# Kernel tuning notes

Hardware: AMD Instinct MI355X
Metric: run time of the kernel (lower is better)

The kernel has to match this reference:

```python
import jax, jax.numpy as jnp
import numpy as np

B, N, C, H, K = 16, 1024, 384, 6, 8
HID = int(C * 2.0)  # mlp_ratio = 2.0
HD = C // H


def _layernorm(x, w, b, eps=1e-5):
    m = x.mean(-1, keepdims=True)
    v = ((x - m) ** 2).mean(-1, keepdims=True)
    return (x - m) * jax.lax.rsqrt(v + eps) * w + b


def setup_inputs() -> dict:
    key = jax.random.key(0)
    ks = jax.random.split(key, 16)
    x = jax.random.normal(ks[0], (B, N, C), jnp.float32)
    # knn indices within each batch, offset by batch*N (as in get_knn_index)
    idx = jax.random.randint(ks[1], (B, K, N), 0, N)
    base = jnp.arange(B, dtype=jnp.int32)[:, None, None] * N
    knn_index = (idx + base).reshape(-1).astype(jnp.int32)
    s = 0.02
    p = {
        "x": x,
        "knn_index": knn_index,
        "ln1_w": jnp.ones((C,), jnp.float32),
        "ln1_b": jnp.zeros((C,), jnp.float32),
        "w_qkv": jax.random.normal(ks[2], (C, 3 * C), jnp.float32) * s,  # qkv_bias=False
        "w_proj": jax.random.normal(ks[3], (C, C), jnp.float32) * s,
        "b_proj": jnp.zeros((C,), jnp.float32),
        "w_knn": jax.random.normal(ks[4], (2 * C, C), jnp.float32) * s,
        "b_knn": jnp.zeros((C,), jnp.float32),
        "w_merge": jax.random.normal(ks[5], (2 * C, C), jnp.float32) * s,
        "b_merge": jnp.zeros((C,), jnp.float32),
        "ln2_w": jnp.ones((C,), jnp.float32),
        "ln2_b": jnp.zeros((C,), jnp.float32),
        "w_fc1": jax.random.normal(ks[6], (C, HID), jnp.float32) * s,
        "b_fc1": jnp.zeros((HID,), jnp.float32),
        "w_fc2": jax.random.normal(ks[7], (HID, C), jnp.float32) * s,
        "b_fc2": jnp.zeros((C,), jnp.float32),
    }
    return p


def reference(x, knn_index, ln1_w, ln1_b, w_qkv, w_proj, b_proj, w_knn, b_knn,
              w_merge, b_merge, ln2_w, ln2_b, w_fc1, b_fc1, w_fc2, b_fc2):
    nx = _layernorm(x, ln1_w, ln1_b)  # [B,N,C]

    # --- self attention ---
    qkv = (nx @ w_qkv).reshape(B, N, 3, H, HD)
    q, k, v = qkv[:, :, 0], qkv[:, :, 1], qkv[:, :, 2]  # [B,N,H,HD]
    scale = HD ** (-0.5)
    attn = jnp.einsum("bnhd,bmhd->bhnm", q, k) * scale
    attn = jax.nn.softmax(attn, axis=-1)
    a_out = jnp.einsum("bhnm,bmhd->bnhd", attn, v).reshape(B, N, C)
    x1 = a_out @ w_proj + b_proj

    # --- graph feature: gather, relative concat, Linear+LeakyReLU, max over k ---
    feat = nx.reshape(B * N, C)[knn_index].reshape(B, K, N, C)
    center = nx[:, None, :, :]  # [B,1,N,C]
    g = jnp.concatenate([feat - center, jnp.broadcast_to(center, (B, K, N, C))], axis=-1)
    knn_f = jax.nn.leaky_relu(g @ w_knn + b_knn, negative_slope=0.2)
    knn_f = knn_f.max(axis=1)  # [B,N,C]

    x1 = jnp.concatenate([x1, knn_f], axis=-1) @ w_merge + b_merge
    x = x + x1

    # --- MLP ---
    h = _layernorm(x, ln2_w, ln2_b)
    h = jax.nn.gelu(h @ w_fc1 + b_fc1, approximate=False) @ w_fc2 + b_fc2
    return x + h
```

## Files before the change

kernel.cpp:

```cpp
#include <hip/hip_runtime.h>
#include <hip/hip_bf16.h>
#include <math.h>

#define BN_ROWS 16384
#define CDIM 384
#define NH 6
#define BBATCH 16
#define NNN 1024

typedef unsigned short u16;
typedef unsigned int u32;
typedef __attribute__((ext_vector_type(8))) short short8;
typedef __attribute__((ext_vector_type(4))) float floatx4;

__device__ __forceinline__ float b2f(u16 s) { return __uint_as_float(((u32)s) << 16); }
__device__ __forceinline__ u16 f2b(float f) {
    __hip_bfloat16 h = __float2bfloat16(f);
    u16 s; __builtin_memcpy(&s, &h, 2); return s;
}
__device__ __forceinline__ void gload_lds16(const u16* g, u16* l) {
    __builtin_amdgcn_global_load_lds(
        (const __attribute__((address_space(1))) unsigned int*)g,
        (__attribute__((address_space(3))) unsigned int*)l, 16, 0, 0);
}

__global__ __launch_bounds__(256) void pack_all(
    const float* __restrict__ W0, u16* __restrict__ T0,
    const float* __restrict__ W1, u16* __restrict__ T1,
    const float* __restrict__ W2, u16* __restrict__ T2,
    const float* __restrict__ W3, u16* __restrict__ T3,
    const float* __restrict__ W4, u16* __restrict__ T4,
    const float* __restrict__ W5, u16* __restrict__ T5)
{
    const float* W; u16* T; int K, N;
    switch (blockIdx.z) {
        case 0: W = W0; T = T0; K = 384; N = 1152; break;
        case 1: W = W1; T = T1; K = 384; N = 384;  break;
        case 2: W = W2; T = T2; K = 768; N = 384;  break;
        case 3: W = W3; T = T3; K = 768; N = 384;  break;
        case 4: W = W4; T = T4; K = 384; N = 768;  break;
        default: W = W5; T = T5; K = 768; N = 384; break;
    }
    const int n0 = blockIdx.x * 32, k0 = blockIdx.y * 32;
    if (n0 >= N || k0 >= K) return;
    __shared__ float s[32][33];
    const int tx = threadIdx.x & 31, ty = threadIdx.x >> 5;
#pragma unroll
    for (int i = 0; i < 4; ++i)
        s[ty + 8 * i][tx] = W[(size_t)(k0 + ty + 8 * i) * N + n0 + tx];
    __syncthreads();
#pragma unroll
    for (int i = 0; i < 4; ++i)
        T[(size_t)(n0 + ty + 8 * i) * K + k0 + tx] = f2b(s[tx][ty + 8 * i]);
}

__global__ __launch_bounds__(64) void ln_kernel(const float* __restrict__ xin,
                                                const float* __restrict__ w,
                                                const float* __restrict__ b,
                                                u16* __restrict__ out)
{
    const int row = blockIdx.x;
    const int t = threadIdx.x;
    const size_t base = (size_t)row * CDIM;
    float v[6];
#pragma unroll
    for (int i = 0; i < 6; ++i) v[i] = xin[base + t + 64 * i];
    float s = 0.f, s2 = 0.f;
#pragma unroll
    for (int i = 0; i < 6; ++i) { s += v[i]; s2 += v[i] * v[i]; }
#pragma unroll
    for (int m = 1; m < 64; m <<= 1) {
        s  += __shfl_xor(s,  m, 64);
        s2 += __shfl_xor(s2, m, 64);
    }
    const float mean = s * (1.0f / CDIM);
    const float var  = s2 * (1.0f / CDIM) - mean * mean;
    const float rs   = rsqrtf(var + 1e-5f);
#pragma unroll
    for (int i = 0; i < 6; ++i) {
        int c = t + 64 * i;
        out[base + c] = f2b((v[i] - mean) * rs * w[c] + b[c]);
    }
}

template<int ACT, bool HAS_BIAS, bool HAS_RES, bool OUT_F32, int MODE, int NT>
__global__ __launch_bounds__(256) void gemm_mfma_kernel(
    const u16* __restrict__ A, int lda,
    const u16* __restrict__ Bt, const u16* __restrict__ Bt2, int ldbt,
    u16* Cb, u16* Cb2, float* Cf, int ldc,
    const float* __restrict__ bias,
    const float* res,
    int K)
{
    constexpr int NTL = NT / 32;
    __shared__ u16 As[128 * 32];
    __shared__ u16 Bs[NT * 32];
    const int tid  = threadIdx.x;
    const int wv   = tid >> 6;
    const int lane = tid & 63;
    const int l15  = lane & 15;
    const int quad = lane >> 4;
    const int m0 = blockIdx.y * 128;
    const int n0 = blockIdx.x * NT;
    const int woffm = (wv >> 1) * 64;
    const int woffn = (wv & 1) * (NT / 2);

    const u16* bsrc = (MODE == 2 && n0 >= 384) ? Bt2 : Bt;
    const int  bn0  = (MODE == 2 && n0 >= 384) ? (n0 - 384) : n0;

    floatx4 acc[4][NTL];
#pragma unroll
    for (int mt = 0; mt < 4; ++mt)
#pragma unroll
        for (int nt = 0; nt < NTL; ++nt) acc[mt][nt] = (floatx4){0.f, 0.f, 0.f, 0.f};

    const int gsw  = 8 * ((lane & 3) ^ ((lane >> 3) & 3));
    const int rloc = lane >> 2;
    const int rdsw = 8 * (quad ^ ((l15 >> 1) & 3));

    for (int kt = 0; kt < K; kt += 32) {
#pragma unroll
        for (int j = 0; j < 2; ++j) {
            const int slab = 32 * wv + 16 * j;
            gload_lds16(A + (size_t)(m0 + slab + rloc) * lda + kt + gsw, &As[slab * 32]);
        }
        if (NT == 128) {
#pragma unroll
            for (int j = 0; j < 2; ++j) {
                const int slab = 32 * wv + 16 * j;
                gload_lds16(bsrc + (size_t)(bn0 + slab + rloc) * ldbt + kt + gsw, &Bs[slab * 32]);
            }
        } else {
            const int slab = 16 * wv;
            gload_lds16(bsrc + (size_t)(bn0 + slab + rloc) * ldbt + kt + gsw, &Bs[slab * 32]);
        }
        __syncthreads();

        short8 af[4], bf[NTL];
#pragma unroll
        for (int mt = 0; mt < 4; ++mt)
            af[mt] = *(const short8*)(As + (woffm + mt * 16 + l15) * 32 + rdsw);
#pragma unroll
        for (int nt = 0; nt < NTL; ++nt)
            bf[nt] = *(const short8*)(Bs + (woffn + nt * 16 + l15) * 32 + rdsw);
#pragma unroll
        for (int mt = 0; mt < 4; ++mt)
#pragma unroll
            for (int nt = 0; nt < NTL; ++nt)
                acc[mt][nt] = __builtin_amdgcn_mfma_f32_16x16x32_bf16(
                    af[mt], bf[nt], acc[mt][nt], 0, 0, 0);
        __syncthreads();
    }

#pragma unroll
    for (int nt = 0; nt < NTL; ++nt) {
        const int gc = n0 + woffn + nt * 16 + l15;
        float bi = 0.f;
        if (HAS_BIAS) bi = bias[gc];
        if (MODE == 2) bi = (gc >= 384) ? bias[gc - 384] : 0.f;
#pragma unroll
        for (int mt = 0; mt < 4; ++mt) {
            const int gr0 = m0 + woffm + mt * 16 + quad * 4;
#pragma unroll
            for (int rr = 0; rr < 4; ++rr) {
                float v = acc[mt][nt][rr] + bi;
                if (ACT == 1) v = 0.5f * v * (1.0f + erff(v * 0.70710678118654752f));
                if (HAS_RES)  v += res[(size_t)(gr0 + rr) * ldc + gc];
                if (MODE == 1) {
                    const int t3  = gc / 384;
                    const int rem = gc - t3 * 384;
                    const int hh = rem >> 6, dd = rem & 63;
                    const int bb = (gr0 + rr) >> 10, nn = (gr0 + rr) & 1023;
                    Cb[((size_t)((bb * 6 + hh) * 1024 + nn)) * 192 + t3 * 64 + dd] = f2b(v);
                } else if (MODE == 2) {
                    if (gc < 384) Cb [(size_t)(gr0 + rr) * 384 + gc]       = f2b(v);
                    else          Cb2[(size_t)(gr0 + rr) * 384 + gc - 384] = f2b(v);
                } else if (OUT_F32) {
                    Cf[(size_t)(gr0 + rr) * ldc + gc] = v;
                } else {
                    Cb[(size_t)(gr0 + rr) * ldc + gc] = f2b(v);
                }
            }
        }
    }
}

__global__ __launch_bounds__(256) void attn_mfma_kernel(const u16* __restrict__ qkv2,
                                                        u16* __restrict__ aout)
{
    const int id = blockIdx.x;
    const int rxcd = id & 7;
    const int j = id >> 3;
    const int slab = rxcd + 8 * (j % 12);
    const int qtile = j / 12;
    const int b = slab / NH, h = slab % NH;

    const int wave = threadIdx.x >> 6;
    const int lane = threadIdx.x & 63;
    const int l15 = lane & 15;
    const int quad = lane >> 4;
    const int qbase = qtile * 128 + wave * 32;
    const int tid = threadIdx.x;

    const u16* slabp = qkv2 + ((size_t)(b * NH + h) << 10) * 192;

    __shared__ __align__(16) u16 Ks[64 * 72];
    __shared__ __align__(16) u16 Vt[64 * 72];
    __shared__ __align__(16) u16 Ps[4][32 * 72];
    __shared__ __align__(16) float Ls[4][32];

    short8 qf[2][2];
#pragma unroll
    for (int nt = 0; nt < 2; ++nt) {
        const u16* qrow = slabp + (size_t)(qbase + nt * 16 + l15) * 192;
        qf[nt][0] = *(const short8*)(qrow + quad * 8);
        qf[nt][1] = *(const short8*)(qrow + 32 + quad * 8);
    }

    float rowsum[2] = {0.f, 0.f};
    floatx4 Oacc[2][4];
#pragma unroll
    for (int mt = 0; mt < 2; ++mt)
#pragma unroll
        for (int nt = 0; nt < 4; ++nt) Oacc[mt][nt] = (floatx4){0.f, 0.f, 0.f, 0.f};

    for (int kc = 0; kc < NNN; kc += 64) {
        {
            const int key = tid >> 2, dblk = (tid & 3) * 16;
            const u16* kp = slabp + (size_t)(kc + key) * 192 + 64 + dblk;
            *(short8*)(Ks + key * 72 + dblk)     = *(const short8*)(kp);
            *(short8*)(Ks + key * 72 + dblk + 8) = *(const short8*)(kp + 8);
        }
        {
            const int kp2 = tid & 31, db = (tid >> 5) * 8;
            const u16* v0p = slabp + (size_t)(kc + 2 * kp2) * 192 + 128 + db;
            uint4 v0 = *(const uint4*)(v0p);
            uint4 v1 = *(const uint4*)(v0p + 192);
            u32 a0[4] = {v0.x, v0.y, v0.z, v0.w};
            u32 a1[4] = {v1.x, v1.y, v1.z, v1.w};
#pragma unroll
            for (int i = 0; i < 8; ++i) {
                u32 w0 = (i & 1) ? (a0[i >> 1] >> 16) : (a0[i >> 1] & 0xffffu);
                u32 w1 = (i & 1) ? (a1[i >> 1] >> 16) : (a1[i >> 1] & 0xffffu);
                *(u32*)(Vt + (size_t)(db + i) * 72 + 2 * kp2) = w0 | (w1 << 16);
            }
        }
        __syncthreads();

        floatx4 sc[4][2];
#pragma unroll
        for (int kt_ = 0; kt_ < 4; ++kt_) {
            short8 kf0 = *(const short8*)(Ks + (kt_ * 16 + l15) * 72 + quad * 8);
            short8 kf1 = *(const short8*)(Ks + (kt_ * 16 + l15) * 72 + 32 + quad * 8);
#pragma unroll
            for (int nt = 0; nt < 2; ++nt) {
                floatx4 s = {0.f, 0.f, 0.f, 0.f};
                s = __builtin_amdgcn_mfma_f32_16x16x32_bf16(kf0, qf[nt][0], s, 0, 0, 0);
                s = __builtin_amdgcn_mfma_f32_16x16x32_bf16(kf1, qf[nt][1], s, 0, 0, 0);
                sc[kt_][nt] = s;
            }
        }

#pragma unroll
        for (int kt_ = 0; kt_ < 4; ++kt_)
#pragma unroll
            for (int nt = 0; nt < 2; ++nt) {
                u16 pk[4];
#pragma unroll
                for (int rr = 0; rr < 4; ++rr) {
                    float p = __expf(sc[kt_][nt][rr] * 0.125f);
                    rowsum[nt] += p;
                    pk[rr] = f2b(p);
                }
                u32 lo = (u32)pk[0] | ((u32)pk[1] << 16);
                u32 hi = (u32)pk[2] | ((u32)pk[3] << 16);
                *(uint2*)(Ps[wave] + (nt * 16 + l15) * 72 + kt_ * 16 + quad * 4) =
                    make_uint2(lo, hi);
            }

        short8 pf[2][2];
#pragma unroll
        for (int mt = 0; mt < 2; ++mt) {
            pf[mt][0] = *(const short8*)(Ps[wave] + (mt * 16 + l15) * 72 + quad * 8);
            pf[mt][1] = *(const short8*)(Ps[wave] + (mt * 16 + l15) * 72 + 32 + quad * 8);
        }
#pragma unroll
        for (int nt = 0; nt < 4; ++nt) {
#pragma unroll
            for (int kk = 0; kk < 2; ++kk) {
                short8 vf = *(const short8*)(Vt + (size_t)(nt * 16 + l15) * 72 + kk * 32 + quad * 8);
#pragma unroll
                for (int mt = 0; mt < 2; ++mt)
                    Oacc[mt][nt] = __builtin_amdgcn_mfma_f32_16x16x32_bf16(
                        pf[mt][kk], vf, Oacc[mt][nt], 0, 0, 0);
            }
        }
        __syncthreads();
    }

#pragma unroll
    for (int nt = 0; nt < 2; ++nt) {
        float l = rowsum[nt];
        l += __shfl_xor(l, 16, 64);
        l += __shfl_xor(l, 32, 64);
        if (quad == 0) Ls[wave][nt * 16 + l15] = l;
    }
#pragma unroll
    for (int mt = 0; mt < 2; ++mt) {
        float4 lv = *(const float4*)&Ls[wave][mt * 16 + quad * 4];
        float li[4] = {lv.x, lv.y, lv.z, lv.w};
#pragma unroll
        for (int rr = 0; rr < 4; ++rr) {
            float inv = 1.0f / li[rr];
            int q = qbase + mt * 16 + quad * 4 + rr;
#pragma unroll
            for (int nt = 0; nt < 4; ++nt)
                aout[(size_t)(b * NNN + q) * CDIM + h * 64 + nt * 16 + l15] =
                    f2b(Oacc[mt][nt][rr] * inv);
        }
    }
}

__global__ __launch_bounds__(128) void knnmax_kernel(const u16* __restrict__ t1,
                                                     const u16* __restrict__ t2,
                                                     const int* __restrict__ idx,
                                                     u16* __restrict__ x1cat)
{
    const int bn = blockIdx.x;
    const int b = bn >> 10, n = bn & 1023;
    int ind[8];
#pragma unroll
    for (int k = 0; k < 8; ++k) ind[k] = idx[b * 8192 + k * 1024 + n];
    const size_t rbase = (size_t)bn * CDIM;
    for (int c = threadIdx.x; c < CDIM; c += 128) {
        float base = b2f(t2[rbase + c]) - b2f(t1[rbase + c]);
        float mx = -1e30f;
#pragma unroll
        for (int k = 0; k < 8; ++k) {
            float v = b2f(t1[(size_t)ind[k] * CDIM + c]) + base;
            v = (v > 0.f) ? v : 0.2f * v;
            mx = fmaxf(mx, v);
        }
        x1cat[(size_t)bn * 768 + CDIM + c] = f2b(mx);
    }
}

extern "C" void kernel_launch(void* const* d_in, const int* in_sizes, int n_in,
                              void* d_out, int out_size, void* d_ws, size_t ws_size,
                              hipStream_t stream)
{
    (void)in_sizes; (void)n_in; (void)out_size; (void)ws_size;
    const float* x     = (const float*)d_in[0];
    const int*   knn   = (const int*)d_in[1];
    const float* ln1w  = (const float*)d_in[2];
    const float* ln1b  = (const float*)d_in[3];
    const float* wqkv  = (const float*)d_in[4];
    const float* wproj = (const float*)d_in[5];
    const float* bproj = (const float*)d_in[6];
    const float* wknn  = (const float*)d_in[7];
    const float* bknn  = (const float*)d_in[8];
    const float* wmrg  = (const float*)d_in[9];
    const float* bmrg  = (const float*)d_in[10];
    const float* ln2w  = (const float*)d_in[11];
    const float* ln2b  = (const float*)d_in[12];
    const float* wfc1  = (const float*)d_in[13];
    const float* bfc1  = (const float*)d_in[14];
    const float* wfc2  = (const float*)d_in[15];
    const float* bfc2  = (const float*)d_in[16];

    u16* wsb = (u16*)d_ws;
    const size_t RE = (size_t)BN_ROWS * CDIM;
    u16* nxb   = wsb;
    u16* qkvb  = wsb + RE;
    u16* x1cat = wsb + RE;
    u16* t1b   = wsb + 3 * RE;
    u16* hinb  = wsb;
    u16* h1b   = wsb + RE;
    u16* wqkvT  = wsb + 4 * RE;
    u16* wprojT = wqkvT + 442368;
    u16* wknnT  = wprojT + 147456;
    u16* wmrgT  = wknnT + 294912;
    u16* wfc1T  = wmrgT + 294912;
    u16* wfc2T  = wfc1T + 294912;
    u16*   aoutb = (u16*)d_out;
    u16*   t2b   = (u16*)d_out;
    float* xmid  = (float*)d_out;

    pack_all<<<dim3(36, 24, 6), 256, 0, stream>>>(
        wqkv, wqkvT, wproj, wprojT, wknn, wknnT, wmrg, wmrgT, wfc1, wfc1T, wfc2, wfc2T);
    ln_kernel<<<BN_ROWS, 64, 0, stream>>>(x, ln1w, ln1b, nxb);
    gemm_mfma_kernel<0, false, false, false, 1, 128><<<dim3(9, 128), 256, 0, stream>>>(
        nxb, CDIM, wqkvT, nullptr, CDIM, qkvb, nullptr, nullptr, 0, nullptr, nullptr, CDIM);
    attn_mfma_kernel<<<768, 256, 0, stream>>>(qkvb, aoutb);
    gemm_mfma_kernel<0, true, false, false, 0, 64><<<dim3(6, 128), 256, 0, stream>>>(
        aoutb, CDIM, wprojT, nullptr, CDIM, x1cat, nullptr, nullptr, 768, bproj, nullptr, CDIM);
    gemm_mfma_kernel<0, false, false, false, 2, 128><<<dim3(6, 128), 256, 0, stream>>>(
        nxb, CDIM, wknnT, wknnT + 384, 768, t1b, t2b, nullptr, CDIM, bknn, nullptr, CDIM);
    knnmax_kernel<<<BN_ROWS, 128, 0, stream>>>(t1b, t2b, knn, x1cat);
    gemm_mfma_kernel<0, true, true, true, 0, 64><<<dim3(6, 128), 256, 0, stream>>>(
        x1cat, 768, wmrgT, nullptr, 768, nullptr, nullptr, xmid, CDIM, bmrg, x, 768);
    ln_kernel<<<BN_ROWS, 64, 0, stream>>>(xmid, ln2w, ln2b, hinb);
    gemm_mfma_kernel<1, true, false, false, 0, 128><<<dim3(6, 128), 256, 0, stream>>>(
        hinb, CDIM, wfc1T, nullptr, CDIM, h1b, nullptr, nullptr, 768, bfc1, nullptr, CDIM);
    gemm_mfma_kernel<0, true, true, true, 0, 64><<<dim3(6, 128), 256, 0, stream>>>(
        h1b, 768, wfc2T, nullptr, 768, nullptr, nullptr, (float*)d_out, CDIM, bfc2, xmid, 768);
}
```

Measured before the change: 346.8 us.

## Double-buffer GEMM LDS tiles and vectorize knn max gather kernel

The MFMA GEMM now uses two LDS buffers for the A and B tiles. It issues the global-to-LDS load for the next K slice before computing on the current one, so memory latency overlaps with the MFMA work and one barrier per iteration is dropped. The knn max kernel now handles two points per block, one wavefront each. Each lane processes 8 channels with 16-byte vector loads and stores. The cost is twice the LDS per GEMM block, which may lower occupancy, and 16 of the 64 lanes in each knn wavefront sit idle.

```diff
diff --git a/kernel.cpp b/kernel.cpp
--- a/kernel.cpp
+++ b/kernel.cpp
@@ -93,8 +93,8 @@
     int K)
 {
     constexpr int NTL = NT / 32;
-    __shared__ u16 As[128 * 32];
-    __shared__ u16 Bs[NT * 32];
+    __shared__ u16 As[2][128 * 32];
+    __shared__ u16 Bs[2][NT * 32];
     const int tid  = threadIdx.x;
     const int wv   = tid >> 6;
     const int lane = tid & 63;
@@ -118,31 +118,37 @@
     const int rloc = lane >> 2;
     const int rdsw = 8 * (quad ^ ((l15 >> 1) & 3));
 
-    for (int kt = 0; kt < K; kt += 32) {
+    auto stage = [&](int kt, int p) {
 #pragma unroll
         for (int j = 0; j < 2; ++j) {
             const int slab = 32 * wv + 16 * j;
-            gload_lds16(A + (size_t)(m0 + slab + rloc) * lda + kt + gsw, &As[slab * 32]);
+            gload_lds16(A + (size_t)(m0 + slab + rloc) * lda + kt + gsw, &As[p][slab * 32]);
         }
         if (NT == 128) {
 #pragma unroll
             for (int j = 0; j < 2; ++j) {
                 const int slab = 32 * wv + 16 * j;
-                gload_lds16(bsrc + (size_t)(bn0 + slab + rloc) * ldbt + kt + gsw, &Bs[slab * 32]);
+                gload_lds16(bsrc + (size_t)(bn0 + slab + rloc) * ldbt + kt + gsw, &Bs[p][slab * 32]);
             }
         } else {
             const int slab = 16 * wv;
-            gload_lds16(bsrc + (size_t)(bn0 + slab + rloc) * ldbt + kt + gsw, &Bs[slab * 32]);
-        }
-        __syncthreads();
+            gload_lds16(bsrc + (size_t)(bn0 + slab + rloc) * ldbt + kt + gsw, &Bs[p][slab * 32]);
+        }
+    };
+
+    stage(0, 0);
+    __syncthreads();
+    int cur = 0;
+    for (int kt = 0; kt < K; kt += 32) {
+        if (kt + 32 < K) stage(kt + 32, cur ^ 1);
 
         short8 af[4], bf[NTL];
 #pragma unroll
         for (int mt = 0; mt < 4; ++mt)
-            af[mt] = *(const short8*)(As + (woffm + mt * 16 + l15) * 32 + rdsw);
+            af[mt] = *(const short8*)(As[cur] + (woffm + mt * 16 + l15) * 32 + rdsw);
 #pragma unroll
         for (int nt = 0; nt < NTL; ++nt)
-            bf[nt] = *(const short8*)(Bs + (woffn + nt * 16 + l15) * 32 + rdsw);
+            bf[nt] = *(const short8*)(Bs[cur] + (woffn + nt * 16 + l15) * 32 + rdsw);
 #pragma unroll
         for (int mt = 0; mt < 4; ++mt)
 #pragma unroll
@@ -150,6 +156,7 @@
                 acc[mt][nt] = __builtin_amdgcn_mfma_f32_16x16x32_bf16(
                     af[mt], bf[nt], acc[mt][nt], 0, 0, 0);
         __syncthreads();
+        cur ^= 1;
     }
 
 #pragma unroll
@@ -326,23 +333,37 @@
                                                      const int* __restrict__ idx,
                                                      u16* __restrict__ x1cat)
 {
-    const int bn = blockIdx.x;
+    const int bn = blockIdx.x * 2 + (threadIdx.x >> 6);
+    const int lane = threadIdx.x & 63;
+    if (lane >= 48) return;
     const int b = bn >> 10, n = bn & 1023;
     int ind[8];
 #pragma unroll
     for (int k = 0; k < 8; ++k) ind[k] = idx[b * 8192 + k * 1024 + n];
-    const size_t rbase = (size_t)bn * CDIM;
-    for (int c = threadIdx.x; c < CDIM; c += 128) {
-        float base = b2f(t2[rbase + c]) - b2f(t1[rbase + c]);
-        float mx = -1e30f;
-#pragma unroll
-        for (int k = 0; k < 8; ++k) {
-            float v = b2f(t1[(size_t)ind[k] * CDIM + c]) + base;
+    const int c0 = lane * 8;
+    const size_t rbase = (size_t)bn * CDIM + c0;
+    short8 v1 = *(const short8*)(t1 + rbase);
+    short8 v2 = *(const short8*)(t2 + rbase);
+    float basef[8], mx[8];
+#pragma unroll
+    for (int j = 0; j < 8; ++j) {
+        basef[j] = b2f((u16)v2[j]) - b2f((u16)v1[j]);
+        mx[j] = -1e30f;
+    }
+#pragma unroll
+    for (int k = 0; k < 8; ++k) {
+        short8 nv = *(const short8*)(t1 + (size_t)ind[k] * CDIM + c0);
+#pragma unroll
+        for (int j = 0; j < 8; ++j) {
+            float v = b2f((u16)nv[j]) + basef[j];
             v = (v > 0.f) ? v : 0.2f * v;
-            mx = fmaxf(mx, v);
-        }
-        x1cat[(size_t)bn * 768 + CDIM + c] = f2b(mx);
-    }
+            mx[j] = fmaxf(mx[j], v);
+        }
+    }
+    short8 ov;
+#pragma unroll
+    for (int j = 0; j < 8; ++j) ov[j] = (short)f2b(mx[j]);
+    *(short8*)(x1cat + (size_t)bn * 768 + CDIM + c0) = ov;
 }
 
 extern "C" void kernel_launch(void* const* d_in, const int* in_sizes, int n_in,
@@ -396,7 +417,7 @@
         aoutb, CDIM, wprojT, nullptr, CDIM, x1cat, nullptr, nullptr, 768, bproj, nullptr, CDIM);
     gemm_mfma_kernel<0, false, false, false, 2, 128><<<dim3(6, 128), 256, 0, stream>>>(
         nxb, CDIM, wknnT, wknnT + 384, 768, t1b, t2b, nullptr, CDIM, bknn, nullptr, CDIM);
-    knnmax_kernel<<<BN_ROWS, 128, 0, stream>>>(t1b, t2b, knn, x1cat);
+    knnmax_kernel<<<BN_ROWS / 2, 128, 0, stream>>>(t1b, t2b, knn, x1cat);
     gemm_mfma_kernel<0, true, true, true, 0, 64><<<dim3(6, 128), 256, 0, stream>>>(
         x1cat, 768, wmrgT, nullptr, 768, nullptr, nullptr, xmid, CDIM, bmrg, x, 768);
     ln_kernel<<<BN_ROWS, 64, 0, stream>>>(xmid, ln2w, ln2b, hinb);
```

Result: no change. 346.8 us (+0.0%).
